# Performance work log

Hardware: AMD Instinct MI355X
Metric: run time of the kernel (lower is better)

The kernel has to match this reference:

```python
import jax, jax.numpy as jnp
import numpy as np

B, S, D, H, M, V, R = 2, 1024, 768, 8, 3072, 32000, 2
HD = D // H  # head_dim = qkv_dim // num_heads


def ln(x, scale, bias, eps=1e-6):
    m = jnp.mean(x, axis=-1, keepdims=True)
    v = jnp.mean(jnp.square(x - m), axis=-1, keepdims=True)
    return (x - m) * jax.lax.rsqrt(v + eps) * scale + bias


def setup_inputs() -> dict:
    key = jax.random.key(0)
    ks = jax.random.split(key, 16)
    r = lambda i, shp, s=0.02: jax.random.normal(ks[i], shp, jnp.float32) * s
    z = lambda shp: jnp.zeros(shp, jnp.float32)
    o = lambda shp: jnp.ones(shp, jnp.float32)
    return {
        'l2r_embed': jax.random.normal(ks[0], (B, S, D), jnp.float32),
        'r2l_embed': jax.random.normal(ks[1], (B, S, D), jnp.float32),
        'temb': jax.random.normal(ks[2], (B, D), jnp.float32),
        'ln_l2r_s': o((D,)), 'ln_l2r_b': z((D,)),
        'ln_r2l_s': o((D,)), 'ln_r2l_b': z((D,)),
        'Wq': r(3, (D, H, HD)), 'bq': z((H, HD)),
        'Wk': r(4, (D, H, HD)), 'bk': z((H, HD)),
        'Wv': r(5, (D, H, HD)), 'bv': z((H, HD)),
        'Wo': r(6, (H, HD, D)), 'bo': z((D,)),
        'ff_ln_s': o((D,)), 'ff_ln_b': z((D,)),
        'ff_w1': r(7, (D, M)), 'ff_b1': z((M,)),
        'ff_w2': r(8, (M, D)), 'ff_b2': z((D,)),
        'tm_w1': r(9, (D, M)), 'tm_b1': z((M,)),
        'tm_w2': r(10, (M, 4 * D)), 'tm_b2': z((4 * D,)),
        'film_w': r(11, (R, 4 * D, 2 * D)), 'film_b': z((R, 2 * D)),
        'r_w1': r(12, (R, D, M)), 'r_b1': z((R, M)),
        'r_w2': r(13, (R, M, D)), 'r_b2': z((R, D)),
        'r_ln_s': o((R, D)), 'r_ln_b': z((R, D)),
        'out_w': r(14, (D, V)), 'out_b': z((V,)),
    }


def reference(l2r_embed, r2l_embed, temb, ln_l2r_s, ln_l2r_b, ln_r2l_s, ln_r2l_b,
              Wq, bq, Wk, bk, Wv, bv, Wo, bo, ff_ln_s, ff_ln_b,
              ff_w1, ff_b1, ff_w2, ff_b2, tm_w1, tm_b1, tm_w2, tm_b2,
              film_w, film_b, r_w1, r_b1, r_w2, r_b2, r_ln_s, r_ln_b,
              out_w, out_b):
    inputs = l2r_embed + r2l_embed
    # prenorm on each direction (temb stays raw)
    l2r_n = ln(l2r_embed, ln_l2r_s, ln_l2r_b)
    r2l_n = ln(r2l_embed, ln_r2l_s, ln_r2l_b)
    # cross attention: query from sum, keys/vals from [temb, l2r, r2l]
    q = jnp.einsum('bsd,dhk->bshk', l2r_n + r2l_n, Wq) + bq
    all_e = jnp.concatenate([temb[:, None, :], l2r_n, r2l_n], axis=1)  # [B, 2S+1, D]
    k = jnp.einsum('bsd,dhk->bshk', all_e, Wk) + bk
    v = jnp.einsum('bsd,dhk->bshk', all_e, Wv) + bv
    q = q / jnp.sqrt(jnp.float32(HD))
    logits = jnp.einsum('bqhd,bkhd->bhqk', q, k)  # [B, H, S, 2S+1]
    idx = jnp.arange(S)
    l2r_mask = idx[:, None] >= idx[None, :]
    r2l_mask = idx[:, None] <= idx[None, :]
    joint = jnp.concatenate(
        [jnp.ones((S, 1), bool), l2r_mask, r2l_mask], axis=-1)[None, None]
    aw = jax.nn.softmax(
        jnp.where(joint, logits, jnp.finfo(jnp.float32).min), axis=-1)
    x = jnp.einsum('bhqk,bkhd->bqhd', aw, v)
    x = jnp.einsum('bqhd,hde->bqe', x, Wo) + bo
    x = x + inputs
    # prenorm FF block
    z = ln(x, ff_ln_s, ff_ln_b)
    z = jax.nn.relu(z @ ff_w1 + ff_b1) @ ff_w2 + ff_b2
    x = x + z
    # residual readout with FiLM conditioning
    t = jax.nn.gelu(temb @ tm_w1 + tm_b1) @ tm_w2 + tm_b2  # [B, 4D]
    for i in range(R):
        film = t @ film_w[i] + film_b[i]  # [B, 2D]
        z = jax.nn.gelu(x @ r_w1[i] + r_b1[i]) @ r_w2[i] + r_b2[i]
        x = ln(x + z, r_ln_s[i], r_ln_b[i])
        a, b = jnp.split(film[:, None, :], 2, axis=-1)
        x = a * x + b
    return x @ out_w + out_b  # [B, S, V]
```

## Files before the change

kernel.cpp:

```cpp
#include <hip/hip_runtime.h>
#include <cstdint>
#include <cstddef>

#define Bb 2
#define Ss 1024
#define Dd 768
#define Hh 8
#define HDh 96
#define Mm 3072
#define Vv 32000
#define KVr 2049

typedef __attribute__((ext_vector_type(8))) short short8v;
typedef __attribute__((ext_vector_type(4))) short short4v;
typedef __attribute__((ext_vector_type(4))) float f32x4;

#define GL16(gp, lp) __builtin_amdgcn_global_load_lds( \
    (const __attribute__((address_space(1))) void*)(gp), \
    (__attribute__((address_space(3))) void*)(lp), 16, 0, 0)

static __device__ __forceinline__ short f2bf(float f) {
  union { float f; unsigned u; } x; x.f = f;
  unsigned r = (x.u + 0x7FFFu + ((x.u >> 16) & 1u)) >> 16;
  return (short)(r & 0xFFFFu);
}

static __device__ __forceinline__ float bf2f(short s) {
  union { unsigned u; float f; } x; x.u = ((unsigned)(unsigned short)s) << 16;
  return x.f;
}

static __device__ __forceinline__ float gelu_f(float v) {
  float u = 0.7978845608028654f * (v + 0.044715f * v * v * v);
  float au = fabsf(u);
  float e = __expf(2.f * au);
  float t = 1.f - 2.f / (e + 1.f);
  return 0.5f * v * (1.f + copysignf(t, u));
}

static __device__ __forceinline__ float blk_sum(float val, float* sh) {
  #pragma unroll
  for (int off = 32; off >= 1; off >>= 1) val += __shfl_xor(val, off);
  __syncthreads();
  if ((threadIdx.x & 63) == 0) sh[threadIdx.x >> 6] = val;
  __syncthreads();
  return sh[0] + sh[1] + sh[2] + sh[3];
}

__global__ __launch_bounds__(256) void prep_kernel(
    const float* __restrict__ l2r, const float* __restrict__ r2l,
    const float* __restrict__ temb,
    const float* __restrict__ s1, const float* __restrict__ b1,
    const float* __restrict__ s2, const float* __restrict__ b2,
    float* __restrict__ inputs, short* __restrict__ all_e)
{
  __shared__ float sh[4];
  const int tid = threadIdx.x;
  if (blockIdx.x >= 2048) {
    int b = blockIdx.x - 2048;
    #pragma unroll
    for (int i = 0; i < 3; ++i)
      all_e[(size_t)b * KVr * Dd + tid + i * 256] = f2bf(temb[(size_t)b * Dd + tid + i * 256]);
    return;
  }
  const int row = blockIdx.x;
  const int b = row >> 10, s = row & 1023;
  const float* ap = l2r + (size_t)row * Dd;
  const float* cp = r2l + (size_t)row * Dd;
  float a0 = ap[tid], a1 = ap[tid + 256], a2 = ap[tid + 512];
  float c0 = cp[tid], c1 = cp[tid + 256], c2 = cp[tid + 512];
  float ma = blk_sum(a0 + a1 + a2, sh) * (1.f / 768.f);
  float mc = blk_sum(c0 + c1 + c2, sh) * (1.f / 768.f);
  float va = blk_sum((a0-ma)*(a0-ma) + (a1-ma)*(a1-ma) + (a2-ma)*(a2-ma), sh) * (1.f / 768.f);
  float vc = blk_sum((c0-mc)*(c0-mc) + (c1-mc)*(c1-mc) + (c2-mc)*(c2-mc), sh) * (1.f / 768.f);
  float ia = rsqrtf(va + 1e-6f), ic = rsqrtf(vc + 1e-6f);
  size_t ro = (size_t)row * Dd;
  size_t e1 = ((size_t)b * KVr + 1 + s) * Dd;
  size_t e2 = ((size_t)b * KVr + 1 + Ss + s) * Dd;
  float av[3] = {a0, a1, a2}, cv[3] = {c0, c1, c2};
  #pragma unroll
  for (int i = 0; i < 3; ++i) {
    int c = tid + i * 256;
    float an = (av[i] - ma) * ia * s1[c] + b1[c];
    float cn = (cv[i] - mc) * ic * s2[c] + b2[c];
    inputs[ro + c] = av[i] + cv[i];
    all_e[e1 + c]  = f2bf(an);
    all_e[e2 + c]  = f2bf(cn);
  }
}

__global__ __launch_bounds__(256) void ln_comb2(
    const float* __restrict__ pk,
    const float* __restrict__ bias, const float* __restrict__ res,
    const float* __restrict__ sc, const float* __restrict__ bi,
    float* __restrict__ yf, short* __restrict__ yb)
{
  __shared__ float sh[4];
  const int row = blockIdx.x, tid = threadIdx.x;
  const size_t PS = (size_t)2048 * 768;
  size_t ro = (size_t)row * Dd;
  float vv[3];
  #pragma unroll
  for (int i = 0; i < 3; ++i) {
    int c = tid + i * 256;
    vv[i] = pk[ro + c] + pk[PS + ro + c] + bias[c] + res[ro + c];
  }
  float m = blk_sum(vv[0] + vv[1] + vv[2], sh) * (1.f / 768.f);
  float var = blk_sum((vv[0]-m)*(vv[0]-m) + (vv[1]-m)*(vv[1]-m) + (vv[2]-m)*(vv[2]-m), sh) * (1.f / 768.f);
  float inv = rsqrtf(var + 1e-6f);
  #pragma unroll
  for (int i = 0; i < 3; ++i) {
    int c = tid + i * 256;
    yf[ro + c] = vv[i];
    yb[ro + c] = f2bf((vv[i] - m) * inv * sc[c] + bi[c]);
  }
}

__global__ __launch_bounds__(256) void ln_comb(
    const float* __restrict__ pk,
    const float* __restrict__ bias, const float* __restrict__ res,
    const float* __restrict__ sc, const float* __restrict__ bi,
    const float* __restrict__ film, float* __restrict__ yf, short* __restrict__ yb)
{
  __shared__ float sh[4];
  const int row = blockIdx.x, tid = threadIdx.x;
  const size_t PS = (size_t)2048 * 768;
  size_t ro = (size_t)row * Dd;
  float vv[3];
  #pragma unroll
  for (int i = 0; i < 3; ++i) {
    int c = tid + i * 256;
    float v = bias[c] + res[ro + c];
    #pragma unroll
    for (int s = 0; s < 4; ++s) v += pk[s * PS + ro + c];
    vv[i] = v;
  }
  float m = blk_sum(vv[0] + vv[1] + vv[2], sh) * (1.f / 768.f);
  float var = blk_sum((vv[0]-m)*(vv[0]-m) + (vv[1]-m)*(vv[1]-m) + (vv[2]-m)*(vv[2]-m), sh) * (1.f / 768.f);
  float inv = rsqrtf(var + 1e-6f);
  int bb = row >> 10;
  #pragma unroll
  for (int i = 0; i < 3; ++i) {
    int c = tid + i * 256;
    float o = (vv[i] - m) * inv * sc[c] + bi[c];
    o = film[(size_t)bb * 1536 + c] * o + film[(size_t)bb * 1536 + 768 + c];
    if (yf) yf[ro + c] = o;
    if (yb) yb[ro + c] = f2bf(o);
  }
}

__global__ __launch_bounds__(256) void combine_kernel(
    const float* __restrict__ pk,
    const float* __restrict__ bias, const float* __restrict__ res,
    float* __restrict__ yf, short* __restrict__ yb)
{
  const int row = blockIdx.x, tid = threadIdx.x;
  const size_t PS = (size_t)2048 * 768;
  size_t ro = (size_t)row * Dd;
  #pragma unroll
  for (int i = 0; i < 3; ++i) {
    int c = tid + i * 256;
    float v = bias[c] + res[ro + c];
    #pragma unroll
    for (int s = 0; s < 4; ++s) v += pk[s * PS + ro + c];
    yf[ro + c] = v;
    yb[ro + c] = f2bf(v);
  }
}

__global__ __launch_bounds__(256) void convT(const float* __restrict__ W, short* __restrict__ Wt,
                                             int K, int N, int ntile)
{
  __shared__ short T[64][72];
  const int bn = blockIdx.x % ntile, bk = blockIdx.x / ntile;
  const int k0 = bk * 64, n0 = bn * 64, tid = threadIdx.x;
  #pragma unroll
  for (int i = 0; i < 4; ++i) {
    int id = i * 256 + tid;
    int r = id >> 4, c4 = (id & 15) * 4;
    float4 w4 = *(const float4*)(W + (size_t)(k0 + r) * N + n0 + c4);
    T[c4 + 0][r] = f2bf(w4.x);
    T[c4 + 1][r] = f2bf(w4.y);
    T[c4 + 2][r] = f2bf(w4.z);
    T[c4 + 3][r] = f2bf(w4.w);
  }
  __syncthreads();
  #pragma unroll
  for (int i = 0; i < 4; ++i) {
    int id = i * 256 + tid;
    int n = id >> 4, k4 = (id & 15) * 4;
    short4v s = *(const short4v*)&T[n][k4];
    *(short4v*)(Wt + (size_t)(n0 + n) * K + k0 + k4) = s;
  }
}

__global__ __launch_bounds__(256) void convT2(const float* __restrict__ W1, short* __restrict__ D1,
                                              const float* __restrict__ W2, short* __restrict__ D2)
{
  __shared__ short T[64][72];
  const int tid = threadIdx.x;
  const bool second = blockIdx.x >= 576;
  const int id576 = second ? (blockIdx.x - 576) : blockIdx.x;
  const int K = second ? 3072 : 768;
  const int N = second ? 768 : 3072;
  const int ntile = N >> 6;
  const float* W = second ? W2 : W1;
  short* Wt = second ? D2 : D1;
  const int bn = id576 % ntile, bk = id576 / ntile;
  const int k0 = bk * 64, n0 = bn * 64;
  #pragma unroll
  for (int i = 0; i < 4; ++i) {
    int id = i * 256 + tid;
    int r = id >> 4, c4 = (id & 15) * 4;
    float4 w4 = *(const float4*)(W + (size_t)(k0 + r) * N + n0 + c4);
    T[c4 + 0][r] = f2bf(w4.x);
    T[c4 + 1][r] = f2bf(w4.y);
    T[c4 + 2][r] = f2bf(w4.z);
    T[c4 + 3][r] = f2bf(w4.w);
  }
  __syncthreads();
  #pragma unroll
  for (int i = 0; i < 4; ++i) {
    int id = i * 256 + tid;
    int n = id >> 4, k4 = (id & 15) * 4;
    short4v s = *(const short4v*)&T[n][k4];
    *(short4v*)(Wt + (size_t)(n0 + n) * K + k0 + k4) = s;
  }
}

__global__ __launch_bounds__(256) void convT4(const float* __restrict__ W0, const float* __restrict__ W1,
                                              const float* __restrict__ W2, const float* __restrict__ W3,
                                              const float* __restrict__ bk, const float* __restrict__ bv,
                                              short* __restrict__ Wt, float* __restrict__ kvb,
                                              const float* __restrict__ part2c, const float* __restrict__ fb,
                                              float* __restrict__ f0, float* __restrict__ f1)
{
  __shared__ short T[64][72];
  const int tid = threadIdx.x;
  if (blockIdx.x >= 577) {
    const int n = (blockIdx.x - 577) * 256 + tid;
    float a0 = fb[n], a1 = a0;
    for (int s = 0; s < 64; ++s) {
      a0 += part2c[(size_t)s * 6144 + n];
      a1 += part2c[(size_t)s * 6144 + 3072 + n];
    }
    float* dst = (n < 1536) ? f0 : f1;
    const int c = (n >= 1536) ? (n - 1536) : n;
    dst[c] = a0;
    dst[1536 + c] = a1;
    return;
  }
  if (blockIdx.x == 576) {
    #pragma unroll
    for (int i = 0; i < 9; ++i) {
      int c = i * 256 + tid;
      if (c < 2304) kvb[c] = (c < 768) ? 0.f : (c < 1536 ? bk[c - 768] : bv[c - 1536]);
    }
    return;
  }
  const int wsel = blockIdx.x / 144, rem = blockIdx.x % 144;
  const float* W = wsel == 0 ? W0 : wsel == 1 ? W1 : wsel == 2 ? W2 : W3;
  short* dst = Wt + (size_t)wsel * 768 * 768;
  const int bn = rem % 12, bk2 = rem / 12;
  const int k0 = bk2 * 64, n0 = bn * 64;
  #pragma unroll
  for (int i = 0; i < 4; ++i) {
    int id = i * 256 + tid;
    int r = id >> 4, c4 = (id & 15) * 4;
    float4 w4 = *(const float4*)(W + (size_t)(k0 + r) * 768 + n0 + c4);
    T[c4 + 0][r] = f2bf(w4.x);
    T[c4 + 1][r] = f2bf(w4.y);
    T[c4 + 2][r] = f2bf(w4.z);
    T[c4 + 3][r] = f2bf(w4.w);
  }
  __syncthreads();
  #pragma unroll
  for (int i = 0; i < 4; ++i) {
    int id = i * 256 + tid;
    int n = id >> 4, k4 = (id & 15) * 4;
    short4v s = *(const short4v*)&T[n][k4];
    *(short4v*)(dst + (size_t)(n0 + n) * 768 + k0 + k4) = s;
  }
}

template<int ACT>
__global__ __launch_bounds__(256, 4) void gemm_bf(
    const short* __restrict__ A, const short* __restrict__ Bt,
    const float* __restrict__ bias, const float* __restrict__ res,
    float* __restrict__ C, short* __restrict__ Cbf, float* __restrict__ Cpart,
    int M, int N, int K, float scale, int mtiles, int ntiles, int ksplit)
{
  __shared__ short As[2][4096];
  __shared__ short Bs[2][4096];
  const int tid = threadIdx.x, lane = tid & 63, wv = tid >> 6;
  const int l15 = lane & 15, l4 = lane >> 4;

  const int nwg = gridDim.x;
  const int qc = nwg >> 3, rc = nwg & 7;
  const int xcd = blockIdx.x & 7, idx = blockIdx.x >> 3;
  const int wgid = (xcd < rc ? xcd * (qc + 1) : rc * (qc + 1) + (xcd - rc) * qc) + idx;
  const int by = wgid % mtiles;
  const int rest = wgid / mtiles;
  const int bx = rest % ntiles;
  const int sp = rest / ntiles;
  const int kper = K / ksplit;
  const int kbeg = sp * kper;
  const int NT = kper >> 5;

  const int m0 = by * 128, n0 = bx * 128;
  const int wm = (wv >> 1) * 64, wn = (wv & 1) * 64;

  const int srow = lane >> 2, schunk = lane & 3;
  const int scsw = (schunk ^ ((srow >> 1) & 3)) << 3;
  const short* sA = A + (size_t)(m0 + wv * 32 + srow) * K + kbeg + scsw;
  const short* sB = Bt + (size_t)(n0 + wv * 32 + srow) * K + kbeg + scsw;
  const int stBase = wv * 1024;
  const int frsw = (l4 ^ ((l15 >> 1) & 3)) << 3;

  f32x4 acc[4][4];
  const f32x4 zz = {0.f, 0.f, 0.f, 0.f};
  #pragma unroll
  for (int i = 0; i < 4; ++i)
    #pragma unroll
    for (int j = 0; j < 4; ++j) acc[i][j] = zz;

  GL16(sA, &As[0][stBase]);
  GL16(sA + (size_t)16 * K, &As[0][stBase + 512]);
  GL16(sB, &Bs[0][stBase]);
  GL16(sB + (size_t)16 * K, &Bs[0][stBase + 512]);

  int buf = 0;
  for (int t = 0; t < NT; ++t) {
    if (t + 1 < NT) {
      int k0 = (t + 1) << 5;
      GL16(sA + k0, &As[buf ^ 1][stBase]);
      GL16(sA + (size_t)16 * K + k0, &As[buf ^ 1][stBase + 512]);
      GL16(sB + k0, &Bs[buf ^ 1][stBase]);
      GL16(sB + (size_t)16 * K + k0, &Bs[buf ^ 1][stBase + 512]);
      asm volatile("s_waitcnt vmcnt(4)" ::: "memory");
    } else {
      asm volatile("s_waitcnt vmcnt(0)" ::: "memory");
    }
    __builtin_amdgcn_s_barrier();

    short8v af[4], bfv[4];
    #pragma unroll
    for (int mi = 0; mi < 4; ++mi)
      af[mi] = *(const short8v*)&As[buf][(wm + mi * 16 + l15) * 32 + frsw];
    #pragma unroll
    for (int ni = 0; ni < 4; ++ni)
      bfv[ni] = *(const short8v*)&Bs[buf][(wn + ni * 16 + l15) * 32 + frsw];
    __builtin_amdgcn_s_setprio(1);
    #pragma unroll
    for (int mi = 0; mi < 4; ++mi)
      #pragma unroll
      for (int ni = 0; ni < 4; ++ni)
        acc[mi][ni] = __builtin_amdgcn_mfma_f32_16x16x32_bf16(af[mi], bfv[ni], acc[mi][ni], 0, 0, 0);
    __builtin_amdgcn_s_setprio(0);
    if (t + 1 < NT) __builtin_amdgcn_s_barrier();
    buf ^= 1;
  }

  if (Cpart) {
    float* Cp = Cpart + (size_t)sp * M * N;
    #pragma unroll
    for (int mi = 0; mi < 4; ++mi)
      #pragma unroll
      for (int r = 0; r < 4; ++r) {
        int row = m0 + wm + mi * 16 + l4 * 4 + r;
        if (row >= M) continue;
        size_t rb = (size_t)row * N;
        #pragma unroll
        for (int ni = 0; ni < 4; ++ni)
          Cp[rb + n0 + wn + ni * 16 + l15] = acc[mi][ni][r];
      }
    return;
  }

  #pragma unroll
  for (int mi = 0; mi < 4; ++mi) {
    #pragma unroll
    for (int r = 0; r < 4; ++r) {
      int row = m0 + wm + mi * 16 + l4 * 4 + r;
      if (row >= M) continue;
      size_t rb = (size_t)row * N;
      #pragma unroll
      for (int ni = 0; ni < 4; ++ni) {
        int col = n0 + wn + ni * 16 + l15;
        float val = (acc[mi][ni][r] + bias[col]) * scale;
        if (ACT == 1) val = fmaxf(val, 0.f);
        if (ACT == 2) val = gelu_f(val);
        if (res) val += res[rb + col];
        if (C)   C[rb + col] = val;
        if (Cbf) Cbf[rb + col] = f2bf(val);
      }
    }
  }
}

__global__ __launch_bounds__(512, 2) void gemm256(
    const short* __restrict__ A, const short* __restrict__ Bt,
    const float* __restrict__ bias, float* __restrict__ C,
    int M, int N, int K, int mtiles)
{
  __shared__ short As[2][16384];
  __shared__ short Bs[2][16384];
  const int tid = threadIdx.x, lane = tid & 63, wv = tid >> 6;
  const int l15 = lane & 15, l4 = lane >> 4;

  const int nwg = gridDim.x;
  const int qc = nwg >> 3, rc = nwg & 7;
  const int xcd = blockIdx.x & 7, idx = blockIdx.x >> 3;
  const int wgid = (xcd < rc ? xcd * (qc + 1) : rc * (qc + 1) + (xcd - rc) * qc) + idx;
  const int by = wgid % mtiles, bx = wgid / mtiles;
  const int m0 = by * 256, n0 = bx * 256;
  const int wm = (wv >> 2) * 128, wn = (wv & 3) * 64;

  const int srow = lane >> 2, schunk = lane & 3;
  const int scsw = (schunk ^ ((srow >> 1) & 3)) << 3;
  const short* sA = A + (size_t)(m0 + wv * 16 + srow) * K + scsw;
  const short* sB = Bt + (size_t)(n0 + wv * 16 + srow) * K + scsw;
  const int stBase = wv * 512;
  const int frsw = (l4 ^ ((l15 >> 1) & 3)) << 3;

  #define STG_A(b, kk, ko) do { \
    GL16(sA + (ko) + (kk) * 32,                  &As[b][(kk) * 8192 + stBase]); \
    GL16(sA + (size_t)128 * K + (ko) + (kk) * 32, &As[b][(kk) * 8192 + 4096 + stBase]); } while (0)
  #define STG_B(b, kk, ko) do { \
    GL16(sB + (ko) + (kk) * 32,                  &Bs[b][(kk) * 8192 + stBase]); \
    GL16(sB + (size_t)128 * K + (ko) + (kk) * 32, &Bs[b][(kk) * 8192 + 4096 + stBase]); } while (0)
  #define ARD(b, kk, row) (*(const short8v*)&As[b][(kk) * 8192 + (row) * 32 + frsw])
  #define BRD(b, kk, row) (*(const short8v*)&Bs[b][(kk) * 8192 + (row) * 32 + frsw])

  f32x4 acc[8][4];
// ... 134 lines not shown
      qf[kk] = tq;
    }
  }

  const f32x4 zz = {0.f, 0.f, 0.f, 0.f};
  f32x4 Oa[6];
  #pragma unroll
  for (int fn = 0; fn < 6; ++fn) Oa[fn] = zz;
  float mrow[4], lrow[4];
  #pragma unroll
  for (int r = 0; r < 4; ++r) { mrow[r] = -3.0e38f; lrow[r] = 0.f; }

  const size_t kvbase = (size_t)b * KVr;

  for (int t = chunk; t < 33; t += 4) {
    int k0 = t * 64;
    bool l2r_vis = (k0 <= Ss) && (k0 - 1 <= qb + 63);
    int rmaxk = (k0 + 63 > 2 * Ss) ? 2 * Ss : (k0 + 63);
    bool r2l_vis = (k0 + 63 >= Ss + 1) && (rmaxk - (Ss + 1) >= qb);
    if (!(t == 0 || l2r_vis || r2l_vis)) continue;

    __syncthreads();
    #pragma unroll
    for (int i = 0; i < 3; ++i) {
      int id = i * 256 + tid;
      int row = id / 12, cc = (id % 12) * 8;
      int key = k0 + row;
      if (key > 2 * Ss) key = 2 * Ss;
      const short* kp = kvq + (kvbase + key) * 2304 + 768 + h * HDh + cc;
      short8v k8 = *(const short8v*)kp;
      *(short8v*)&Kls[row][cc] = k8;
      short8v v8 = *(const short8v*)(kp + 768);
      #pragma unroll
      for (int j = 0; j < 8; ++j) Vt[cc + j][row] = v8[j];
    }
    __syncthreads();

    f32x4 sc[4];
    #pragma unroll
    for (int nt = 0; nt < 4; ++nt) {
      f32x4 d = zz;
      #pragma unroll
      for (int kk = 0; kk < 3; ++kk) {
        short8v kf = *(const short8v*)&Kls[nt * 16 + l15][kk * 32 + l4 * 8];
        d = __builtin_amdgcn_mfma_f32_16x16x32_bf16(qf[kk], kf, d, 0, 0, 0);
      }
      sc[nt] = d;
    }
    float tmax[4] = {-3.0e38f, -3.0e38f, -3.0e38f, -3.0e38f};
    #pragma unroll
    for (int nt = 0; nt < 4; ++nt)
      #pragma unroll
      for (int r = 0; r < 4; ++r) {
        int qg = qw + l4 * 4 + r;
        int j = k0 + nt * 16 + l15;
        bool vis = (j == 0) ||
                   (j >= 1 && j <= Ss && (j - 1) <= qg) ||
                   (j >= Ss + 1 && j <= 2 * Ss && (j - (Ss + 1)) >= qg);
        if (!vis) sc[nt][r] = -3.0e38f;
        tmax[r] = fmaxf(tmax[r], sc[nt][r]);
      }
    #pragma unroll
    for (int r = 0; r < 4; ++r) {
      #pragma unroll
      for (int off = 8; off >= 1; off >>= 1) tmax[r] = fmaxf(tmax[r], __shfl_xor(tmax[r], off));
    }
    float scl[4];
    #pragma unroll
    for (int r = 0; r < 4; ++r) {
      float mnew = fmaxf(mrow[r], tmax[r]);
      scl[r] = __expf(mrow[r] - mnew);
      mrow[r] = mnew;
    }
    #pragma unroll
    for (int fn = 0; fn < 6; ++fn)
      #pragma unroll
      for (int r = 0; r < 4; ++r) Oa[fn][r] *= scl[r];
    float lad[4] = {0.f, 0.f, 0.f, 0.f};
    #pragma unroll
    for (int nt = 0; nt < 4; ++nt)
      #pragma unroll
      for (int r = 0; r < 4; ++r) {
        float p = __expf(sc[nt][r] - mrow[r]);
        lad[r] += p;
        Pls[w][l4 * 4 + r][nt * 16 + l15] = f2bf(p);
      }
    #pragma unroll
    for (int r = 0; r < 4; ++r) {
      #pragma unroll
      for (int off = 8; off >= 1; off >>= 1) lad[r] += __shfl_xor(lad[r], off);
      lrow[r] = lrow[r] * scl[r] + lad[r];
    }
    __syncthreads();

    short8v pf[2];
    #pragma unroll
    for (int kk = 0; kk < 2; ++kk) pf[kk] = *(const short8v*)&Pls[w][l15][kk * 32 + l4 * 8];
    #pragma unroll
    for (int fn = 0; fn < 6; ++fn) {
      #pragma unroll
      for (int kk = 0; kk < 2; ++kk) {
        short8v vf = *(const short8v*)&Vt[fn * 16 + l15][kk * 32 + l4 * 8];
        Oa[fn] = __builtin_amdgcn_mfma_f32_16x16x32_bf16(pf[kk], vf, Oa[fn], 0, 0, 0);
      }
    }
  }

  float* Op = (chunk == 0) ? Op0 : (chunk == 1) ? Op1 : (chunk == 2) ? Op2 : Op3;
  #pragma unroll
  for (int fn = 0; fn < 6; ++fn)
    #pragma unroll
    for (int r = 0; r < 4; ++r) {
      int row = qw + l4 * 4 + r;
      int col = h * HDh + fn * 16 + l15;
      Op[((size_t)(b * Ss + row)) * Dd + col] = Oa[fn][r];
    }
  if (l15 == 0) {
    #pragma unroll
    for (int r = 0; r < 4; ++r) {
      int row = qw + l4 * 4 + r;
      size_t ix = (size_t)chunk * 32768 + (((size_t)(b * 8 + h) * 1024 + row) * 2);
      ml[ix] = mrow[r];
      ml[ix + 1] = lrow[r];
    }
  }
}

__global__ __launch_bounds__(256) void attn_merge(
    const float* __restrict__ Op0, const float* __restrict__ Op1,
    const float* __restrict__ Op2, const float* __restrict__ Op3,
    const float* __restrict__ ml, short* __restrict__ o)
{
  const int row = blockIdx.x, tid = threadIdx.x;
  const int b = row >> 10, s = row & 1023;
  size_t ro = (size_t)row * Dd;
  #pragma unroll
  for (int i = 0; i < 3; ++i) {
    int c = tid + i * 256;
    int h = c / HDh;
    size_t ix = ((size_t)(b * 8 + h) * 1024 + s) * 2;
    float m0 = ml[ix], l0 = ml[ix + 1];
    float m1 = ml[32768 + ix], l1 = ml[32768 + ix + 1];
    float m2 = ml[65536 + ix], l2 = ml[65536 + ix + 1];
    float m3 = ml[98304 + ix], l3 = ml[98304 + ix + 1];
    float mm = fmaxf(fmaxf(m0, m1), fmaxf(m2, m3));
    float s0 = __expf(m0 - mm), s1 = __expf(m1 - mm);
    float s2 = __expf(m2 - mm), s3 = __expf(m3 - mm);
    float denom = s0 * l0 + s1 * l1 + s2 * l2 + s3 * l3;
    float val = s0 * Op0[ro + c] + s1 * Op1[ro + c] + s2 * Op2[ro + c] + s3 * Op3[ro + c];
    o[ro + c] = f2bf(val / denom);
  }
}

__global__ __launch_bounds__(256) void thin1(const float* __restrict__ A, const float* __restrict__ W,
                                             float* __restrict__ part, int K, int N, int nblk, int splits)
{
  __shared__ float a0s[64], a1s[64];
  const int nb = blockIdx.x % nblk, ks = blockIdx.x / nblk;
  const int kl = K / splits, kbeg = ks * kl;
  const int tid = threadIdx.x;
  for (int k = tid; k < kl; k += 256) { a0s[k] = A[kbeg + k]; a1s[k] = A[K + kbeg + k]; }
  __syncthreads();
  const int n = nb * 256 + tid;
  float acc0 = 0.f, acc1 = 0.f;
  for (int k = 0; k < kl; ++k) {
    float w = W[(size_t)(kbeg + k) * N + n];
    acc0 = fmaf(a0s[k], w, acc0);
    acc1 = fmaf(a1s[k], w, acc1);
  }
  part[(size_t)ks * 2 * N + n] = acc0;
  part[(size_t)ks * 2 * N + N + n] = acc1;
}

__global__ __launch_bounds__(256) void thin1p(
    const float* __restrict__ pin, const float* __restrict__ bin,
    const float* __restrict__ W, float* __restrict__ part)
{
  __shared__ float a0s[48], a1s[48];
  const int nb = blockIdx.x % 12, ks = blockIdx.x / 12;
  const int kbeg = ks * 48, tid = threadIdx.x;
  for (int j = tid; j < 96; j += 256) {
    int row = j / 48, k = j % 48;
    float v = bin[kbeg + k];
    for (int s = 0; s < 64; ++s) v += pin[(size_t)s * 6144 + (size_t)row * 3072 + kbeg + k];
    v = gelu_f(v);
    if (row) a1s[k] = v; else a0s[k] = v;
  }
  __syncthreads();
  const int n = nb * 256 + tid;
  float acc0 = 0.f, acc1 = 0.f;
  for (int k = 0; k < 48; ++k) {
    float w = W[(size_t)(kbeg + k) * 3072 + n];
    acc0 = fmaf(a0s[k], w, acc0);
    acc1 = fmaf(a1s[k], w, acc1);
  }
  part[(size_t)ks * 6144 + n] = acc0;
  part[(size_t)ks * 6144 + 3072 + n] = acc1;
}

__global__ __launch_bounds__(256) void film1p(
    const float* __restrict__ pin, const float* __restrict__ bin,
    const float* __restrict__ W, float* __restrict__ part)
{
  __shared__ float a0s[48], a1s[48];
  const int nb = blockIdx.x % 12, ks = blockIdx.x / 12;
  const int kbeg = ks * 48, tid = threadIdx.x;
  for (int j = tid; j < 96; j += 256) {
    int row = j / 48, k = j % 48;
    float v = bin[kbeg + k];
    for (int s = 0; s < 64; ++s) v += pin[(size_t)s * 6144 + (size_t)row * 3072 + kbeg + k];
    if (row) a1s[k] = v; else a0s[k] = v;
  }
  __syncthreads();
  const int n = nb * 256 + tid;
  const int col = (n >= 1536) ? (n - 1536) : n;
  const float* Wp = W + ((n < 1536) ? (size_t)0 : (size_t)3072 * 1536)
                      + (size_t)kbeg * 1536 + col;
  float acc0 = 0.f, acc1 = 0.f;
  for (int k = 0; k < 48; ++k) {
    float w = Wp[(size_t)k * 1536];
    acc0 = fmaf(a0s[k], w, acc0);
    acc1 = fmaf(a1s[k], w, acc1);
  }
  part[(size_t)ks * 6144 + n] = acc0;
  part[(size_t)ks * 6144 + 3072 + n] = acc1;
}

static void gemm_launch(int act, const short* A, const short* Bt, const float* bias,
                        const float* res, float* C, short* Cbf, float* Cpart,
                        int M, int N, int K, float scale, int ksplit, hipStream_t s)
{
  int mt = (M + 127) >> 7, nt = N >> 7;
  dim3 grid(mt * nt * ksplit), blk(256);
  if (act == 1)      gemm_bf<1><<<grid, blk, 0, s>>>(A, Bt, bias, res, C, Cbf, Cpart, M, N, K, scale, mt, nt, ksplit);
  else if (act == 2) gemm_bf<2><<<grid, blk, 0, s>>>(A, Bt, bias, res, C, Cbf, Cpart, M, N, K, scale, mt, nt, ksplit);
  else               gemm_bf<0><<<grid, blk, 0, s>>>(A, Bt, bias, res, C, Cbf, Cpart, M, N, K, scale, mt, nt, ksplit);
}

static void conv_launch(const float* W, short* Wt, int K, int N, hipStream_t s)
{
  int nt = N >> 6, kt = K >> 6;
  convT<<<dim3(nt * kt), dim3(256), 0, s>>>(W, Wt, K, N, nt);
}

extern "C" void kernel_launch(void* const* d_in, const int* in_sizes, int n_in,
                              void* d_out, int out_size, void* d_ws, size_t ws_size,
                              hipStream_t stream)
{
  (void)in_sizes; (void)n_in; (void)out_size; (void)ws_size;
  const float* l2r      = (const float*)d_in[0];
  const float* r2l      = (const float*)d_in[1];
  const float* temb     = (const float*)d_in[2];
  const float* ln_l2r_s = (const float*)d_in[3];
  const float* ln_l2r_b = (const float*)d_in[4];
  const float* ln_r2l_s = (const float*)d_in[5];
  const float* ln_r2l_b = (const float*)d_in[6];
  const float* Wq = (const float*)d_in[7];
  const float* bq = (const float*)d_in[8];
  const float* Wk = (const float*)d_in[9];
  const float* bk = (const float*)d_in[10];
  const float* Wv = (const float*)d_in[11];
  const float* bv = (const float*)d_in[12];
  const float* Wo = (const float*)d_in[13];
  const float* bo = (const float*)d_in[14];
  const float* ff_ln_s = (const float*)d_in[15];
  const float* ff_ln_b = (const float*)d_in[16];
  const float* ff_w1 = (const float*)d_in[17];
  const float* ff_b1 = (const float*)d_in[18];
  const float* ff_w2 = (const float*)d_in[19];
  const float* ff_b2 = (const float*)d_in[20];
  const float* tm_w1 = (const float*)d_in[21];
  const float* tm_b1 = (const float*)d_in[22];
  const float* tm_w2 = (const float*)d_in[23];
  const float* tm_b2 = (const float*)d_in[24];
  const float* film_w = (const float*)d_in[25];
  const float* film_b = (const float*)d_in[26];
  const float* r_w1 = (const float*)d_in[27];
  const float* r_b1 = (const float*)d_in[28];
  const float* r_w2 = (const float*)d_in[29];
  const float* r_b2 = (const float*)d_in[30];
  const float* r_ln_s = (const float*)d_in[31];
  const float* r_ln_b = (const float*)d_in[32];
  const float* out_w = (const float*)d_in[33];
  const float* out_b = (const float*)d_in[34];

  uint8_t* base = (uint8_t*)d_ws;
  short* alle_bf = (short*)(base + 3145728);
  short* kvq     = (short*)(base + 9440256);
  short* attn_bf = (short*)(base + 12585984);
  float* inputs  = (float*)(base + 28323840);
  float* xbuf    = (float*)(base + 34615296);
  short* xn_bf   = (short*)(base + 40906752);
  short* big_bf  = (short*)(base + 44052480);
  float* x2f     = (float*)(base + 56635392);
  short* x2bf    = (short*)(base + 62926848);
  float* x3f     = (float*)(base + 66072576);
  short* x3bf    = (short*)(base + 72364032);
  short* x4bf    = (short*)(base + 75509760);
  short* wslot   = (short*)(base + 78655488);
  uint8_t* sm    = base + 83374080;
  float* f0    = (float*)(sm + 0);
  float* f1    = (float*)(sm + 12288);
  float* kvbia = (float*)(sm + 24576);
  short* w2slot = (short*)inputs;
  float* part2a = (float*)(base + 44052480);
  float* part2b = (float*)(base + 44052480 + 1572864);
  float* part2c = (float*)(base + 44052480 + 3145728);
  float* Op0 = (float*)(base + 3145728);
  float* Op1 = xbuf;
  float* Op2 = (float*)(base + 44052480);
  float* Op3 = (float*)(base + 50343936);
  float* mlb = (float*)(base + 56635392);
  float* wopart = (float*)(base + 44052480);
  float* partK = (float*)(base + 0);
  short* outwT = (short*)(base + 0);

  dim3 blk(256);

  thin1<<<dim3(12 * 64), blk, 0, stream>>>(temb, tm_w1, part2a, 768, 3072, 12, 64);
  thin1p<<<dim3(12 * 64), blk, 0, stream>>>(part2a, tm_b1, tm_w2, part2b);
  film1p<<<dim3(12 * 64), blk, 0, stream>>>(part2b, tm_b2, film_w, part2c);

  prep_kernel<<<2050, blk, 0, stream>>>(l2r, r2l, temb, ln_l2r_s, ln_l2r_b, ln_r2l_s, ln_r2l_b,
                                        inputs, alle_bf);

  convT4<<<dim3(589), blk, 0, stream>>>(Wq, Wk, Wv, Wo, bk, bv, wslot, kvbia,
                                        part2c, film_b, f0, f1);

  gemm_launch(0, alle_bf, wslot, kvbia, nullptr, nullptr, kvq, nullptr, 4098, 2304, 768, 1.f, 1, stream);

  attn_kernel<<<1024, blk, 0, stream>>>(kvq, bq, Op0, Op1, Op2, Op3, mlb);
  attn_merge<<<2048, blk, 0, stream>>>(Op0, Op1, Op2, Op3, mlb, attn_bf);

  gemm_launch(0, attn_bf, wslot + (size_t)3 * 768 * 768, bo, nullptr, nullptr, nullptr, wopart, 2048, 768, 768, 1.f, 2, stream);
  ln_comb2<<<2048, blk, 0, stream>>>(wopart, bo, inputs, ff_ln_s, ff_ln_b, xbuf, xn_bf);

  convT2<<<dim3(1152), blk, 0, stream>>>(ff_w1, wslot, ff_w2, w2slot);
  gemm_launch(1, xn_bf, wslot, ff_b1, nullptr, nullptr, big_bf, nullptr, 2048, 3072, 768, 1.f, 1, stream);
  gemm_launch(0, big_bf, w2slot, nullptr, nullptr, nullptr, nullptr, partK, 2048, 768, 3072, 1.f, 4, stream);
  combine_kernel<<<2048, blk, 0, stream>>>(partK, ff_b2, xbuf, x2f, x2bf);

  convT2<<<dim3(1152), blk, 0, stream>>>(r_w1, wslot, r_w2, w2slot);
  gemm_launch(2, x2bf, wslot, r_b1, nullptr, nullptr, big_bf, nullptr, 2048, 3072, 768, 1.f, 1, stream);
  gemm_launch(0, big_bf, w2slot, nullptr, nullptr, nullptr, nullptr, partK, 2048, 768, 3072, 1.f, 4, stream);
  ln_comb<<<2048, blk, 0, stream>>>(partK, r_b2, x2f, r_ln_s, r_ln_b, f0, x3f, x3bf);

  convT2<<<dim3(1152), blk, 0, stream>>>(r_w1 + (size_t)768 * 3072, wslot,
                                         r_w2 + (size_t)3072 * 768, w2slot);
  gemm_launch(2, x3bf, wslot, r_b1 + 3072, nullptr, nullptr, big_bf, nullptr, 2048, 3072, 768, 1.f, 1, stream);
  gemm_launch(0, big_bf, w2slot, nullptr, nullptr, nullptr, nullptr, partK, 2048, 768, 3072, 1.f, 4, stream);
  ln_comb<<<2048, blk, 0, stream>>>(partK, r_b2 + 768, x3f, r_ln_s + 768, r_ln_b + 768, f1, nullptr, x4bf);

  conv_launch(out_w, outwT, 768, 32000, stream);
  gemm256<<<dim3(8 * 125), dim3(512), 0, stream>>>(x4bf, outwT, out_b, (float*)d_out,
                                                   2048, 32000, 768, 8);
}
```

Before: 532.8 us.

## Merge small kernels: cooperative temb path, fuse weight conversions into row kernels

The three temb/FiLM matvec kernels become one cooperative kernel that uses grid.sync between stages. The Q/K/V/O weight conversion is folded into the prep kernel, and the per-layer weight transposes are folded into the combine and LN-combine kernels as extra blocks. The aim is to cut kernel-launch count and let conversion blocks overlap with row-wise work. The cooperative launch needs all 768 blocks to be co-resident, and its return status is not checked.

```diff
diff --git a/kernel.cpp b/kernel.cpp
--- a/kernel.cpp
+++ b/kernel.cpp
@@ -1,6 +1,9 @@
 #include <hip/hip_runtime.h>
+#include <hip/hip_cooperative_groups.h>
 #include <cstdint>
 #include <cstddef>
+
+namespace cg = cooperative_groups;
 
 #define Bb 2
 #define Ss 1024
@@ -47,15 +50,144 @@
   return sh[0] + sh[1] + sh[2] + sh[3];
 }
 
-__global__ __launch_bounds__(256) void prep_kernel(
+__global__ __launch_bounds__(256) void tpath_coop(
+    const float* __restrict__ temb,
+    const float* __restrict__ tm_w1, const float* __restrict__ tm_b1,
+    const float* __restrict__ tm_w2, const float* __restrict__ tm_b2,
+    const float* __restrict__ film_w, const float* __restrict__ film_b,
+    float* __restrict__ part2a, float* __restrict__ part2b, float* __restrict__ part2c,
+    float* __restrict__ f0, float* __restrict__ f1)
+{
+  cg::grid_group grid = cg::this_grid();
+  __shared__ float a0s[48], a1s[48];
+  const int tid = threadIdx.x;
+  const int nb = blockIdx.x % 12, ks = blockIdx.x / 12;
+  const int n = nb * 256 + tid;
+
+  {
+    const int kbeg = ks * 12;
+    for (int k = tid; k < 12; k += 256) { a0s[k] = temb[kbeg + k]; a1s[k] = temb[768 + kbeg + k]; }
+    __syncthreads();
+    float acc0 = 0.f, acc1 = 0.f;
+    for (int k = 0; k < 12; ++k) {
+      float w = tm_w1[(size_t)(kbeg + k) * 3072 + n];
+      acc0 = fmaf(a0s[k], w, acc0);
+      acc1 = fmaf(a1s[k], w, acc1);
+    }
+    part2a[(size_t)ks * 6144 + n] = acc0;
+    part2a[(size_t)ks * 6144 + 3072 + n] = acc1;
+  }
+  grid.sync();
+
+  {
+    const int kbeg = ks * 48;
+    for (int j = tid; j < 96; j += 256) {
+      int row = j / 48, k = j % 48;
+      float v = tm_b1[kbeg + k];
+      for (int s = 0; s < 64; ++s) v += part2a[(size_t)s * 6144 + (size_t)row * 3072 + kbeg + k];
+      v = gelu_f(v);
+      if (row) a1s[k] = v; else a0s[k] = v;
+    }
+    __syncthreads();
+    float acc0 = 0.f, acc1 = 0.f;
+    for (int k = 0; k < 48; ++k) {
+      float w = tm_w2[(size_t)(kbeg + k) * 3072 + n];
+      acc0 = fmaf(a0s[k], w, acc0);
+      acc1 = fmaf(a1s[k], w, acc1);
+    }
+    part2b[(size_t)ks * 6144 + n] = acc0;
+    part2b[(size_t)ks * 6144 + 3072 + n] = acc1;
+  }
+  grid.sync();
+
+  {
+    const int kbeg = ks * 48;
+    for (int j = tid; j < 96; j += 256) {
+      int row = j / 48, k = j % 48;
+      float v = tm_b2[kbeg + k];
+      for (int s = 0; s < 64; ++s) v += part2b[(size_t)s * 6144 + (size_t)row * 3072 + kbeg + k];
+      if (row) a1s[k] = v; else a0s[k] = v;
+    }
+    __syncthreads();
+    const int col = (n >= 1536) ? (n - 1536) : n;
+    const float* Wp = film_w + ((n < 1536) ? (size_t)0 : (size_t)3072 * 1536)
+                             + (size_t)kbeg * 1536 + col;
+    float acc0 = 0.f, acc1 = 0.f;
+    for (int k = 0; k < 48; ++k) {
+      float w = Wp[(size_t)k * 1536];
+      acc0 = fmaf(a0s[k], w, acc0);
+      acc1 = fmaf(a1s[k], w, acc1);
+    }
+    part2c[(size_t)ks * 6144 + n] = acc0;
+    part2c[(size_t)ks * 6144 + 3072 + n] = acc1;
+  }
+  grid.sync();
+
+  if (blockIdx.x < 12) {
+    const int nn = blockIdx.x * 256 + tid;
+    float a0 = film_b[nn], a1 = a0;
+    for (int s = 0; s < 64; ++s) {
+      a0 += part2c[(size_t)s * 6144 + nn];
+      a1 += part2c[(size_t)s * 6144 + 3072 + nn];
+    }
+    float* dst = (nn < 1536) ? f0 : f1;
+    const int c = (nn >= 1536) ? (nn - 1536) : nn;
+    dst[c] = a0;
+    dst[1536 + c] = a1;
+  }
+}
+
+__global__ __launch_bounds__(256) void prep_conv(
     const float* __restrict__ l2r, const float* __restrict__ r2l,
     const float* __restrict__ temb,
     const float* __restrict__ s1, const float* __restrict__ b1,
     const float* __restrict__ s2, const float* __restrict__ b2,
-    float* __restrict__ inputs, short* __restrict__ all_e)
+    float* __restrict__ inputs, short* __restrict__ all_e,
+    const float* __restrict__ W0, const float* __restrict__ W1,
+    const float* __restrict__ W2, const float* __restrict__ W3,
+    const float* __restrict__ bk, const float* __restrict__ bv,
+    short* __restrict__ Wt, float* __restrict__ kvb)
 {
   __shared__ float sh[4];
+  __shared__ short T[64][72];
   const int tid = threadIdx.x;
+
+  if (blockIdx.x >= 2050) {
+    const int cb = blockIdx.x - 2050;
+    if (cb == 576) {
+      #pragma unroll
+      for (int i = 0; i < 9; ++i) {
+        int c = i * 256 + tid;
+        if (c < 2304) kvb[c] = (c < 768) ? 0.f : (c < 1536 ? bk[c - 768] : bv[c - 1536]);
+      }
+      return;
+    }
+    const int wsel = cb / 144, rem = cb % 144;
+    const float* W = wsel == 0 ? W0 : wsel == 1 ? W1 : wsel == 2 ? W2 : W3;
+    short* dst = Wt + (size_t)wsel * 768 * 768;
+    const int bn = rem % 12, bk2 = rem / 12;
+    const int k0 = bk2 * 64, n0 = bn * 64;
+    #pragma unroll
+    for (int i = 0; i < 4; ++i) {
+      int id = i * 256 + tid;
+      int r = id >> 4, c4 = (id & 15) * 4;
+      float4 w4 = *(const float4*)(W + (size_t)(k0 + r) * 768 + n0 + c4);
+      T[c4 + 0][r] = f2bf(w4.x);
+      T[c4 + 1][r] = f2bf(w4.y);
+      T[c4 + 2][r] = f2bf(w4.z);
+      T[c4 + 3][r] = f2bf(w4.w);
+    }
+    __syncthreads();
+    #pragma unroll
+    for (int i = 0; i < 4; ++i) {
+      int id = i * 256 + tid;
+      int nn = id >> 4, k4 = (id & 15) * 4;
+      short4v s = *(const short4v*)&T[nn][k4];
+      *(short4v*)(dst + (size_t)(n0 + nn) * 768 + k0 + k4) = s;
+    }
+    return;
+  }
+
   if (blockIdx.x >= 2048) {
     int b = blockIdx.x - 2048;
     #pragma unroll
@@ -149,12 +281,46 @@
   }
 }
 
-__global__ __launch_bounds__(256) void combine_kernel(
-    const float* __restrict__ pk,
-    const float* __restrict__ bias, const float* __restrict__ res,
-    float* __restrict__ yf, short* __restrict__ yb)
-{
-  const int row = blockIdx.x, tid = threadIdx.x;
+__global__ __launch_bounds__(256) void comb_convT2(
+    const float* __restrict__ pk, const float* __restrict__ bias, const float* __restrict__ res,
+    float* __restrict__ yf, short* __restrict__ yb,
+    const float* __restrict__ W1, short* __restrict__ D1,
+    const float* __restrict__ W2, short* __restrict__ D2)
+{
+  const int tid = threadIdx.x;
+  if (blockIdx.x >= 2048) {
+    __shared__ short T[64][72];
+    const int id = blockIdx.x - 2048;
+    const bool second = id >= 576;
+    const int id576 = second ? (id - 576) : id;
+    const int K = second ? 3072 : 768;
+    const int N = second ? 768 : 3072;
+    const int ntile = N >> 6;
+    const float* W = second ? W2 : W1;
+    short* Wt = second ? D2 : D1;
+    const int bn = id576 % ntile, bk = id576 / ntile;
+    const int k0 = bk * 64, n0 = bn * 64;
+    #pragma unroll
+    for (int i = 0; i < 4; ++i) {
+      int jd = i * 256 + tid;
+      int r = jd >> 4, c4 = (jd & 15) * 4;
+      float4 w4 = *(const float4*)(W + (size_t)(k0 + r) * N + n0 + c4);
+      T[c4 + 0][r] = f2bf(w4.x);
+      T[c4 + 1][r] = f2bf(w4.y);
+      T[c4 + 2][r] = f2bf(w4.z);
+      T[c4 + 3][r] = f2bf(w4.w);
+    }
+    __syncthreads();
+    #pragma unroll
+    for (int i = 0; i < 4; ++i) {
+      int jd = i * 256 + tid;
+      int nn = jd >> 4, k4 = (jd & 15) * 4;
+      short4v s = *(const short4v*)&T[nn][k4];
+      *(short4v*)(Wt + (size_t)(n0 + nn) * K + k0 + k4) = s;
+    }
+    return;
+  }
+  const int row = blockIdx.x;
   const size_t PS = (size_t)2048 * 768;
   size_t ro = (size_t)row * Dd;
   #pragma unroll
@@ -165,6 +331,73 @@
     for (int s = 0; s < 4; ++s) v += pk[s * PS + ro + c];
     yf[ro + c] = v;
     yb[ro + c] = f2bf(v);
+  }
+}
+
+__global__ __launch_bounds__(256) void lncomb_convT2(
+    const float* __restrict__ pk, const float* __restrict__ bias, const float* __restrict__ res,
+    const float* __restrict__ sc, const float* __restrict__ bi,
+    const float* __restrict__ film, float* __restrict__ yf, short* __restrict__ yb,
+    const float* __restrict__ W1, short* __restrict__ D1,
+    const float* __restrict__ W2, short* __restrict__ D2)
+{
+  const int tid = threadIdx.x;
+  if (blockIdx.x >= 2048) {
+    __shared__ short T[64][72];
+    const int id = blockIdx.x - 2048;
+    const bool second = id >= 576;
+    const int id576 = second ? (id - 576) : id;
+    const int K = second ? 3072 : 768;
+    const int N = second ? 768 : 3072;
+    const int ntile = N >> 6;
+    const float* W = second ? W2 : W1;
+    short* Wt = second ? D2 : D1;
+    const int bn = id576 % ntile, bk = id576 / ntile;
+    const int k0 = bk * 64, n0 = bn * 64;
+    #pragma unroll
+    for (int i = 0; i < 4; ++i) {
+      int jd = i * 256 + tid;
+      int r = jd >> 4, c4 = (jd & 15) * 4;
+      float4 w4 = *(const float4*)(W + (size_t)(k0 + r) * N + n0 + c4);
+      T[c4 + 0][r] = f2bf(w4.x);
+      T[c4 + 1][r] = f2bf(w4.y);
+      T[c4 + 2][r] = f2bf(w4.z);
+      T[c4 + 3][r] = f2bf(w4.w);
+    }
+    __syncthreads();
+    #pragma unroll
+    for (int i = 0; i < 4; ++i) {
+      int jd = i * 256 + tid;
+      int nn = jd >> 4, k4 = (jd & 15) * 4;
+      short4v s = *(const short4v*)&T[nn][k4];
+      *(short4v*)(Wt + (size_t)(n0 + nn) * K + k0 + k4) = s;
+    }
+    return;
+  }
+  __shared__ float sh[4];
+  const int row = blockIdx.x;
+  const size_t PS = (size_t)2048 * 768;
+  size_t ro = (size_t)row * Dd;
+  float vv[3];
+  #pragma unroll
+  for (int i = 0; i < 3; ++i) {
+    int c = tid + i * 256;
+    float v = bias[c] + res[ro + c];
+    #pragma unroll
+    for (int s = 0; s < 4; ++s) v += pk[s * PS + ro + c];
+    vv[i] = v;
+  }
+  float m = blk_sum(vv[0] + vv[1] + vv[2], sh) * (1.f / 768.f);
+  float var = blk_sum((vv[0]-m)*(vv[0]-m) + (vv[1]-m)*(vv[1]-m) + (vv[2]-m)*(vv[2]-m), sh) * (1.f / 768.f);
+  float inv = rsqrtf(var + 1e-6f);
+  int bb = row >> 10;
+  #pragma unroll
+  for (int i = 0; i < 3; ++i) {
+    int c = tid + i * 256;
+    float o = (vv[i] - m) * inv * sc[c] + bi[c];
+    o = film[(size_t)bb * 1536 + c] * o + film[(size_t)bb * 1536 + 768 + c];
+    yf[ro + c] = o;
+    yb[ro + c] = f2bf(o);
   }
 }
 
@@ -225,61 +458,6 @@
     int n = id >> 4, k4 = (id & 15) * 4;
     short4v s = *(const short4v*)&T[n][k4];
     *(short4v*)(Wt + (size_t)(n0 + n) * K + k0 + k4) = s;
-  }
-}
-
-__global__ __launch_bounds__(256) void convT4(const float* __restrict__ W0, const float* __restrict__ W1,
-                                              const float* __restrict__ W2, const float* __restrict__ W3,
-                                              const float* __restrict__ bk, const float* __restrict__ bv,
-                                              short* __restrict__ Wt, float* __restrict__ kvb,
-                                              const float* __restrict__ part2c, const float* __restrict__ fb,
-                                              float* __restrict__ f0, float* __restrict__ f1)
-{
-  __shared__ short T[64][72];
-  const int tid = threadIdx.x;
-  if (blockIdx.x >= 577) {
-    const int n = (blockIdx.x - 577) * 256 + tid;
-    float a0 = fb[n], a1 = a0;
-    for (int s = 0; s < 64; ++s) {
-      a0 += part2c[(size_t)s * 6144 + n];
-      a1 += part2c[(size_t)s * 6144 + 3072 + n];
-    }
-    float* dst = (n < 1536) ? f0 : f1;
-    const int c = (n >= 1536) ? (n - 1536) : n;
-    dst[c] = a0;
-    dst[1536 + c] = a1;
-    return;
-  }
-  if (blockIdx.x == 576) {
-    #pragma unroll
-    for (int i = 0; i < 9; ++i) {
-      int c = i * 256 + tid;
-      if (c < 2304) kvb[c] = (c < 768) ? 0.f : (c < 1536 ? bk[c - 768] : bv[c - 1536]);
-    }
-    return;
-  }
-  const int wsel = blockIdx.x / 144, rem = blockIdx.x % 144;
-  const float* W = wsel == 0 ? W0 : wsel == 1 ? W1 : wsel == 2 ? W2 : W3;
-  short* dst = Wt + (size_t)wsel * 768 * 768;
-  const int bn = rem % 12, bk2 = rem / 12;
-  const int k0 = bk2 * 64, n0 = bn * 64;
-  #pragma unroll
-  for (int i = 0; i < 4; ++i) {
-    int id = i * 256 + tid;
-    int r = id >> 4, c4 = (id & 15) * 4;
-    float4 w4 = *(const float4*)(W + (size_t)(k0 + r) * 768 + n0 + c4);
-    T[c4 + 0][r] = f2bf(w4.x);
-    T[c4 + 1][r] = f2bf(w4.y);
-    T[c4 + 2][r] = f2bf(w4.z);
-    T[c4 + 3][r] = f2bf(w4.w);
-  }
-  __syncthreads();
-  #pragma unroll
-  for (int i = 0; i < 4; ++i) {
-    int id = i * 256 + tid;
-    int n = id >> 4, k4 = (id & 15) * 4;
-    short4v s = *(const short4v*)&T[n][k4];
-    *(short4v*)(dst + (size_t)(n0 + n) * 768 + k0 + k4) = s;
   }
 }
 
@@ -720,80 +898,6 @@
   }
 }
 
-__global__ __launch_bounds__(256) void thin1(const float* __restrict__ A, const float* __restrict__ W,
-                                             float* __restrict__ part, int K, int N, int nblk, int splits)
-{
-  __shared__ float a0s[64], a1s[64];
-  const int nb = blockIdx.x % nblk, ks = blockIdx.x / nblk;
-  const int kl = K / splits, kbeg = ks * kl;
-  const int tid = threadIdx.x;
-  for (int k = tid; k < kl; k += 256) { a0s[k] = A[kbeg + k]; a1s[k] = A[K + kbeg + k]; }
-  __syncthreads();
-  const int n = nb * 256 + tid;
-  float acc0 = 0.f, acc1 = 0.f;
-  for (int k = 0; k < kl; ++k) {
-    float w = W[(size_t)(kbeg + k) * N + n];
-    acc0 = fmaf(a0s[k], w, acc0);
-    acc1 = fmaf(a1s[k], w, acc1);
-  }
-  part[(size_t)ks * 2 * N + n] = acc0;
-  part[(size_t)ks * 2 * N + N + n] = acc1;
-}
-
-__global__ __launch_bounds__(256) void thin1p(
-    const float* __restrict__ pin, const float* __restrict__ bin,
-    const float* __restrict__ W, float* __restrict__ part)
-{
-  __shared__ float a0s[48], a1s[48];
-  const int nb = blockIdx.x % 12, ks = blockIdx.x / 12;
-  const int kbeg = ks * 48, tid = threadIdx.x;
-  for (int j = tid; j < 96; j += 256) {
-    int row = j / 48, k = j % 48;
-    float v = bin[kbeg + k];
-    for (int s = 0; s < 64; ++s) v += pin[(size_t)s * 6144 + (size_t)row * 3072 + kbeg + k];
-    v = gelu_f(v);
-    if (row) a1s[k] = v; else a0s[k] = v;
-  }
-  __syncthreads();
-  const int n = nb * 256 + tid;
-  float acc0 = 0.f, acc1 = 0.f;
-  for (int k = 0; k < 48; ++k) {
-    float w = W[(size_t)(kbeg + k) * 3072 + n];
-    acc0 = fmaf(a0s[k], w, acc0);
-    acc1 = fmaf(a1s[k], w, acc1);
-  }
-  part[(size_t)ks * 6144 + n] = acc0;
-  part[(size_t)ks * 6144 + 3072 + n] = acc1;
-}
-
-__global__ __launch_bounds__(256) void film1p(
-    const float* __restrict__ pin, const float* __restrict__ bin,
-    const float* __restrict__ W, float* __restrict__ part)
-{
-  __shared__ float a0s[48], a1s[48];
-  const int nb = blockIdx.x % 12, ks = blockIdx.x / 12;
-  const int kbeg = ks * 48, tid = threadIdx.x;
-  for (int j = tid; j < 96; j += 256) {
-    int row = j / 48, k = j % 48;
-    float v = bin[kbeg + k];
-    for (int s = 0; s < 64; ++s) v += pin[(size_t)s * 6144 + (size_t)row * 3072 + kbeg + k];
-    if (row) a1s[k] = v; else a0s[k] = v;
-  }
-  __syncthreads();
-  const int n = nb * 256 + tid;
-  const int col = (n >= 1536) ? (n - 1536) : n;
-  const float* Wp = W + ((n < 1536) ? (size_t)0 : (size_t)3072 * 1536)
-                      + (size_t)kbeg * 1536 + col;
-  float acc0 = 0.f, acc1 = 0.f;
-  for (int k = 0; k < 48; ++k) {
-    float w = Wp[(size_t)k * 1536];
-    acc0 = fmaf(a0s[k], w, acc0);
-    acc1 = fmaf(a1s[k], w, acc1);
-  }
-  part[(size_t)ks * 6144 + n] = acc0;
-  part[(size_t)ks * 6144 + 3072 + n] = acc1;
-}
-
 static void gemm_launch(int act, const short* A, const short* Bt, const float* bias,
                         const float* res, float* C, short* Cbf, float* Cpart,
                         int M, int N, int K, float scale, int ksplit, hipStream_t s)
@@ -803,12 +907,6 @@
   if (act == 1)      gemm_bf<1><<<grid, blk, 0, s>>>(A, Bt, bias, res, C, Cbf, Cpart, M, N, K, scale, mt, nt, ksplit);
   else if (act == 2) gemm_bf<2><<<grid, blk, 0, s>>>(A, Bt, bias, res, C, Cbf, Cpart, M, N, K, scale, mt, nt, ksplit);
   else               gemm_bf<0><<<grid, blk, 0, s>>>(A, Bt, bias, res, C, Cbf, Cpart, M, N, K, scale, mt, nt, ksplit);
-}
-
-static void conv_launch(const float* W, short* Wt, int K, int N, hipStream_t s)
-{
-  int nt = N >> 6, kt = K >> 6;
-  convT<<<dim3(nt * kt), dim3(256), 0, s>>>(W, Wt, K, N, nt);
 }
 
 extern "C" void kernel_launch(void* const* d_in, const int* in_sizes, int n_in,
@@ -885,41 +983,44 @@
 
   dim3 blk(256);
 
-  thin1<<<dim3(12 * 64), blk, 0, stream>>>(temb, tm_w1, part2a, 768, 3072, 12, 64);
-  thin1p<<<dim3(12 * 64), blk, 0, stream>>>(part2a, tm_b1, tm_w2, part2b);
-  film1p<<<dim3(12 * 64), blk, 0, stream>>>(part2b, tm_b2, film_w, part2c);
-
-  prep_kernel<<<2050, blk, 0, stream>>>(l2r, r2l, temb, ln_l2r_s, ln_l2r_b, ln_r2l_s, ln_r2l_b,
-                                        inputs, alle_bf);
-
-  convT4<<<dim3(589), blk, 0, stream>>>(Wq, Wk, Wv, Wo, bk, bv, wslot, kvbia,
-                                        part2c, film_b, f0, f1);
+  {
+    void* args[] = { (void*)&temb, (void*)&tm_w1, (void*)&tm_b1, (void*)&tm_w2, (void*)&tm_b2,
+                     (void*)&film_w, (void*)&film_b,
+                     (void*)&part2a, (void*)&part2b, (void*)&part2c, (void*)&f0, (void*)&f1 };
+    hipLaunchCooperativeKernel((const void*)tpath_coop, dim3(768), blk, args, 0, stream);
+  }
+
+  prep_conv<<<dim3(2627), blk, 0, stream>>>(l2r, r2l, temb, ln_l2r_s, ln_l2r_b, ln_r2l_s, ln_r2l_b,
+                                            inputs, alle_bf, Wq, Wk, Wv, Wo, bk, bv, wslot, kvbia);
 
   gemm_launch(0, alle_bf, wslot, kvbia, nullptr, nullptr, kvq, nullptr, 4098, 2304, 768, 1.f, 1, stream);
 
-  attn_kernel<<<1024, blk, 0, stream>>>(kvq, bq, Op0, Op1, Op2, Op3, mlb);
-  attn_merge<<<2048, blk, 0, stream>>>(Op0, Op1, Op2, Op3, mlb, attn_bf);
+  attn_kernel<<<dim3(1024), blk, 0, stream>>>(kvq, bq, Op0, Op1, Op2, Op3, mlb);
+  attn_merge<<<dim3(2048), blk, 0, stream>>>(Op0, Op1, Op2, Op3, mlb, attn_bf);
 
   gemm_launch(0, attn_bf, wslot + (size_t)3 * 768 * 768, bo, nullptr, nullptr, nullptr, wopart, 2048, 768, 768, 1.f, 2, stream);
-  ln_comb2<<<2048, blk, 0, stream>>>(wopart, bo, inputs, ff_ln_s, ff_ln_b, xbuf, xn_bf);
+  ln_comb2<<<dim3(2048), blk, 0, stream>>>(wopart, bo, inputs, ff_ln_s, ff_ln_b, xbuf, xn_bf);
 
   convT2<<<dim3(1152), blk, 0, stream>>>(ff_w1, wslot, ff_w2, w2slot);
   gemm_launch(1, xn_bf, wslot, ff_b1, nullptr, nullptr, big_bf, nullptr, 2048, 3072, 768, 1.f, 1, stream);
   gemm_launch(0, big_bf, w2slot, nullptr, nullptr, nullptr, nullptr, partK, 2048, 768, 3072, 1.f, 4, stream);
-  combine_kernel<<<2048, blk, 0, stream>>>(partK, ff_b2, xbuf, x2f, x2bf);
-
-  convT2<<<dim3(1152), blk, 0, stream>>>(r_w1, wslot, r_w2, w2slot);
+
+  comb_convT2<<<dim3(3200), blk, 0, stream>>>(partK, ff_b2, xbuf, x2f, x2bf,
+                                              r_w1, wslot, r_w2, w2slot);
+
   gemm_launch(2, x2bf, wslot, r_b1, nullptr, nullptr, big_bf, nullptr, 2048, 3072, 768, 1.f, 1, stream);
   gemm_launch(0, big_bf, w2slot, nullptr, nullptr, nullptr, nullptr, partK, 2048, 768, 3072, 1.f, 4, stream);
-  ln_comb<<<2048, blk, 0, stream>>>(partK, r_b2, x2f, r_ln_s, r_ln_b, f0, x3f, x3bf);
-
-  convT2<<<dim3(1152), blk, 0, stream>>>(r_w1 + (size_t)768 * 3072, wslot,
-                                         r_w2 + (size_t)3072 * 768, w2slot);
+
+  lncomb_convT2<<<dim3(3200), blk, 0, stream>>>(partK, r_b2, x2f, r_ln_s, r_ln_b, f0, x3f, x3bf,
+                                                r_w1 + (size_t)768 * 3072, wslot,
+                                                r_w2 + (size_t)3072 * 768, w2slot);
+
   gemm_launch(2, x3bf, wslot, r_b1 + 3072, nullptr, nullptr, big_bf, nullptr, 2048, 3072, 768, 1.f, 1, stream);
   gemm_launch(0, big_bf, w2slot, nullptr, nullptr, nullptr, nullptr, partK, 2048, 768, 3072, 1.f, 4, stream);
-  ln_comb<<<2048, blk, 0, stream>>>(partK, r_b2 + 768, x3f, r_ln_s + 768, r_ln_b + 768, f1, nullptr, x4bf);
-
-  conv_launch(out_w, outwT, 768, 32000, stream);
+
+  ln_comb<<<dim3(2048), blk, 0, stream>>>(partK, r_b2 + 768, x3f, r_ln_s + 768, r_ln_b + 768, f1, nullptr, x4bf);
+
+  convT<<<dim3(6000), blk, 0, stream>>>(out_w, outwT, 768, 32000, 500);
   gemm256<<<dim3(8 * 125), dim3(512), 0, stream>>>(x4bf, outwT, out_b, (float*)d_out,
                                                    2048, 32000, 768, 8);
 }
```

Result: slower. 749.2 us (+40.6%).
